# Performance work log

Hardware: AMD Instinct MI355X
Metric: run time of the kernel (lower is better)

Reference implementation:

```python
import jax, jax.numpy as jnp
import numpy as np

T = 5  # frames per clip, hardcoded in the module
H = 8  # heads


def _to_heads(z, b, n_, h, dh):
    # '(b t) n (h d) -> b h (n t) d' with t=T
    z = z.reshape(b, T, n_, h, dh)
    z = z.transpose(0, 3, 2, 1, 4)  # b h n t d
    return z.reshape(b, h, n_ * T, dh)


def _from_heads(z, b, n_, h, dh):
    # 'b h (n t) d -> (b t) n (h d)'
    z = z.reshape(b, h, n_, T, dh)
    z = z.transpose(0, 3, 2, 1, 4)  # b t n h d
    return z.reshape(b * T, n_, h * dh)


def setup_inputs() -> dict:
    key = jax.random.key(0)
    ks = jax.random.split(key, 6)
    bt, n, dim = 160, 257, 512
    inner = 512
    x = jax.random.normal(ks[0], (bt, n, dim), dtype=jnp.float32)
    mask = jax.random.uniform(ks[1], (bt, 16, 16), dtype=jnp.float32)
    Wv_qkv = jax.random.normal(ks[2], (dim, inner * 3), dtype=jnp.float32) * (dim ** -0.5)
    Wa_qkv = jax.random.normal(ks[3], (dim, inner * 3), dtype=jnp.float32) * (dim ** -0.5)
    Wo = jax.random.normal(ks[4], (inner, dim), dtype=jnp.float32) * (inner ** -0.5)
    bo = jnp.zeros((dim,), dtype=jnp.float32)
    return {"x": x, "mask": mask, "Wv_qkv": Wv_qkv, "Wa_qkv": Wa_qkv, "Wo": Wo, "bo": bo}


def reference(x, mask, Wv_qkv, Wa_qkv, Wo, bo):
    bt, n, dim = x.shape
    b = bt // T
    h = H
    inner = Wv_qkv.shape[1] // 3
    dh = inner // h
    scale = dh ** -0.5

    A = x[:, :1]   # (bt, 1, dim)
    V = x[:, 1:]   # (bt, n-1, dim)

    v_qkv = jnp.split(V @ Wv_qkv, 3, axis=-1)
    a_qkv = jnp.split(A @ Wa_qkv, 3, axis=-1)
    qv, kv, vv = (_to_heads(z, b, n - 1, h, dh) for z in v_qkv)  # (b,h,(n-1)*T,dh)
    qa, ka, va = (_to_heads(z, b, 1, h, dh) for z in a_qkv)       # (b,h,T,dh)

    # multiplicative query mask: (bt,16,16) -> (bt, n-1, 1) broadcast to dim -> heads layout
    m = jnp.broadcast_to(mask.reshape(bt, n - 1, 1), (bt, n - 1, h * dh))
    m = _to_heads(m, b, n - 1, h, dh)
    qv = qv * m

    # audio queries attend over visual keys/values
    av_dots = jnp.einsum('bhqd,bhkd->bhqk', qa, kv) * scale  # (b,h,T,(n-1)*T)
    av_out = jnp.einsum('bhqk,bhkd->bhqd', jax.nn.softmax(av_dots, axis=-1), vv)

    # visual queries attend over audio keys/values
    va_dots = jnp.einsum('bhqd,bhkd->bhqk', qv, ka) * scale  # (b,h,(n-1)*T,T)
    va_out = jnp.einsum('bhqk,bhkd->bhqd', jax.nn.softmax(va_dots, axis=-1), va)

    a_out = _from_heads(av_out, b, 1, h, dh)      # (bt, 1, inner)
    v_out = _from_heads(va_out, b, n - 1, h, dh)  # (bt, n-1, inner)
    out = jnp.concatenate((a_out, v_out), axis=1)  # (bt, n, inner)
    return out @ Wo + bo
```

## Files before the change

kernel.cpp:

```cpp
#include <hip/hip_runtime.h>
#include <hip/hip_bf16.h>

typedef unsigned short u16;
typedef __bf16 bf16x8 __attribute__((ext_vector_type(8)));
typedef u16 u16x8 __attribute__((ext_vector_type(8)));
typedef float f32x4 __attribute__((ext_vector_type(4)));

__device__ __forceinline__ float bf2f(u16 u) {
    return __uint_as_float(((unsigned)u) << 16);
}
__device__ __forceinline__ u16 f2bf(float f) {
    unsigned u = __float_as_uint(f);
    unsigned r = (u + 0x7fffu + ((u >> 16) & 1u)) >> 16;
    return (u16)r;
}

__device__ __forceinline__ void gl_lds16(const u16* g, u16* l) {
    __builtin_amdgcn_global_load_lds(
        (const __attribute__((address_space(1))) void*)g,
        (__attribute__((address_space(3))) void*)l, 16, 0, 0);
}

__global__ __launch_bounds__(256) void prep(const float* __restrict__ x,
                                            const float* __restrict__ Wv,
                                            const float* __restrict__ Wa,
                                            const float* __restrict__ Wo,
                                            u16* __restrict__ xb,
                                            u16* __restrict__ WvTv,
                                            u16* __restrict__ WaT,
                                            u16* __restrict__ WoT) {
    __shared__ float tile[64][65];
    int blk = blockIdx.x;
    if (blk < 10280) {
        int i = (blk * 256 + threadIdx.x) * 8;
        float4 a = *(const float4*)&x[i];
        float4 b = *(const float4*)&x[i + 4];
        u16x8 o;
        o[0] = f2bf(a.x); o[1] = f2bf(a.y); o[2] = f2bf(a.z); o[3] = f2bf(a.w);
        o[4] = f2bf(b.x); o[5] = f2bf(b.y); o[6] = f2bf(b.z); o[7] = f2bf(b.w);
        *(u16x8*)&xb[i] = o;
        return;
    }
    blk -= 10280;
    const float* W; u16* WT; int N, stride, coff;
    if (blk < 64)       { W = Wv; WT = WvTv; N = 512;  stride = 1536; coff = 1024; }
    else if (blk < 256) { W = Wa; WT = WaT;  N = 1536; stride = 1536; coff = 0; blk -= 64; }
    else                { W = Wo; WT = WoT;  N = 512;  stride = 512;  coff = 0; blk -= 256; }
    const int nt = N >> 6;
    const int k0 = (blk / nt) << 6;
    const int n0 = (blk % nt) << 6;
    for (int i = threadIdx.x; i < 4096; i += 256) {
        int r = i >> 6, c = i & 63;
        tile[r][c] = W[(size_t)(k0 + r) * stride + coff + n0 + c];
    }
    __syncthreads();
    for (int i = threadIdx.x; i < 4096; i += 256) {
        int r = i >> 6, c = i & 63;
        WT[(size_t)(n0 + r) * 512 + k0 + c] = f2bf(tile[c][r]);
    }
}

template <int MODE, int OUTF>
__global__ __launch_bounds__(256) void gemm_k(const u16* __restrict__ A,
                                              const u16* __restrict__ Bt,
                                              void* __restrict__ Cv,
                                              const float* __restrict__ bias,
                                              int M, int N, int K) {
    __shared__ u16 As[128][64];
    __shared__ u16 Bs[128][64];
    const int t = threadIdx.x;
    const int bn0 = blockIdx.x * 128;
    const int bm0 = blockIdx.y * 128;
    const int wave = t >> 6, lane = t & 63;
    const int wm = (wave >> 1) * 64, wn = (wave & 1) * 64;
    const int lr = lane & 15, lh = lane >> 4;
    const int srow = wave * 8 + (lane >> 3);
    const int scol = (lane & 7) * 8;

    f32x4 acc[4][4] = {};

    for (int kt = 0; kt < K; kt += 64) {
        __syncthreads();
#pragma unroll
        for (int i = 0; i < 4; i++) {
            int row = i * 32 + srow;
            int r = bm0 + row;
            long g;
            if (MODE == 0) g = (r < M) ? (long)r : 0l;
            else           g = (r < M) ? (long)r * 257 : 0l;
            gl_lds16(&A[g * K + kt + scol], &As[0][0] + i * 2048 + wave * 512);
            long nr = bn0 + row;
            gl_lds16(&Bt[nr * K + kt + scol], &Bs[0][0] + i * 2048 + wave * 512);
        }
        __syncthreads();
#pragma unroll
        for (int kk = 0; kk < 2; kk++) {
            bf16x8 af[4], bfr[4];
#pragma unroll
            for (int mi = 0; mi < 4; mi++)
                af[mi] = *(const bf16x8*)&As[wm + mi * 16 + lr][kk * 32 + lh * 8];
#pragma unroll
            for (int ni = 0; ni < 4; ni++)
                bfr[ni] = *(const bf16x8*)&Bs[wn + ni * 16 + lr][kk * 32 + lh * 8];
#pragma unroll
            for (int mi = 0; mi < 4; mi++)
#pragma unroll
                for (int ni = 0; ni < 4; ni++)
                    acc[mi][ni] = __builtin_amdgcn_mfma_f32_16x16x32_bf16(
                        af[mi], bfr[ni], acc[mi][ni], 0, 0, 0);
        }
    }

#pragma unroll
    for (int mi = 0; mi < 4; mi++)
#pragma unroll
        for (int ni = 0; ni < 4; ni++)
#pragma unroll
            for (int r2 = 0; r2 < 4; r2++) {
                int m = bm0 + wm + mi * 16 + lh * 4 + r2;
                if (m < M) {
                    int nc = bn0 + wn + ni * 16 + lr;
                    float v = acc[mi][ni][r2];
                    if (OUTF == 2)      ((float*)Cv)[(size_t)m * 257 * N + nc] = v + bias[nc];
                    else                ((u16*)Cv)[(size_t)m * N + nc] = f2bf(v);
                }
            }
}

__global__ __launch_bounds__(1024) void gemm_vs(const u16* __restrict__ A,
                                                const u16* __restrict__ WvTv,
                                                const u16* __restrict__ wcomb,
                                                u16* __restrict__ vv,
                                                float* __restrict__ pglob,
                                                float* __restrict__ vascore) {
    __shared__ u16 As[2][256][64];
    __shared__ u16 Bs[2][256][64];
    const int t = threadIdx.x;
    const int nwg = gridDim.x;
    const int orig = blockIdx.x;
    const int qc = nwg >> 3;
    const int xcd = orig & 7, slot = orig >> 3;
    const int wgid = xcd * qc + slot;
    const int my = wgid / 3, sec = wgid % 3;
    const int bm0 = my * 256;
    const int bt = my, b = bt / 5, t5 = bt - b * 5;
    const int bn0 = (sec < 2) ? sec * 256 : 0;
    const u16* Bt = (sec < 2) ? WvTv : (wcomb + (size_t)b * 256 * 512);
    const int wave = t >> 6, lane = t & 63;
    const int wm = (wave >> 2) * 64, wn = (wave & 3) * 64;
    const int lr = lane & 15, lh = lane >> 4;
    const int xr = (lr & 7) << 3;
    const bool active = (sec < 2) || (wn < 128);
    u16* AsF = &As[0][0][0];
    u16* BsF = &Bs[0][0][0];

    const int gsa = ((lane & 7) ^ (lane >> 3)) * 8;
    auto stage = [&](int buf, int kt_) {
        const int kc = kt_ * 64;
#pragma unroll
        for (int j = 0; j < 2; j++) {
            int c0 = j * 1024 + wave * 64;
            int row = (c0 + lane) >> 3;
            int r = bm0 + row;
            long ga = (long)(r >> 8) * 257 + (r & 255) + 1;
            gl_lds16(&A[ga * 512 + kc + gsa], AsF + buf * 16384 + c0 * 8);
            gl_lds16(&Bt[(long)(bn0 + row) * 512 + kc + gsa], BsF + buf * 16384 + c0 * 8);
        }
    };

    f32x4 acc[4][4] = {};

    stage(0, 0);
    __builtin_amdgcn_sched_barrier(0);
    stage(1, 1);
    __builtin_amdgcn_sched_barrier(0);
    asm volatile("s_waitcnt vmcnt(0)" ::: "memory");
    __builtin_amdgcn_s_barrier();
    __builtin_amdgcn_sched_barrier(0);

    int cur = 0;
    for (int kt = 0; kt < 8; kt++) {
        if (active) {
            __builtin_amdgcn_s_setprio(1);
#pragma unroll
            for (int kk = 0; kk < 2; kk++) {
                bf16x8 af[4], bfr[4];
#pragma unroll
                for (int mi = 0; mi < 4; mi++)
                    af[mi] = *(const bf16x8*)&As[cur][wm + mi * 16 + lr][(kk * 32 + lh * 8) ^ xr];
#pragma unroll
                for (int ni = 0; ni < 4; ni++)
                    bfr[ni] = *(const bf16x8*)&Bs[cur][wn + ni * 16 + lr][(kk * 32 + lh * 8) ^ xr];
#pragma unroll
                for (int mi = 0; mi < 4; mi++)
#pragma unroll
                    for (int ni = 0; ni < 4; ni++)
                        acc[mi][ni] = __builtin_amdgcn_mfma_f32_16x16x32_bf16(
                            af[mi], bfr[ni], acc[mi][ni], 0, 0, 0);
            }
            __builtin_amdgcn_s_setprio(0);
        }
        if (kt == 7) break;
        __builtin_amdgcn_sched_barrier(0);
        __builtin_amdgcn_s_barrier();
        __builtin_amdgcn_sched_barrier(0);
        if (kt + 2 < 8) {
            stage(cur, kt + 2);
            __builtin_amdgcn_sched_barrier(0);
            asm volatile("s_waitcnt vmcnt(4)" ::: "memory");
        } else {
            asm volatile("s_waitcnt vmcnt(0)" ::: "memory");
        }
        __builtin_amdgcn_sched_barrier(0);
        __builtin_amdgcn_s_barrier();
        __builtin_amdgcn_sched_barrier(0);
        cur ^= 1;
    }

    if (sec < 2) {
#pragma unroll
        for (int mi = 0; mi < 4; mi++)
#pragma unroll
            for (int ni = 0; ni < 4; ni++)
#pragma unroll
                for (int r2 = 0; r2 < 4; r2++) {
                    int m = bm0 + wm + mi * 16 + lh * 4 + r2;
                    int nc = bn0 + wn + ni * 16 + lr;
                    vv[(size_t)m * 512 + nc] = f2bf(acc[mi][ni][r2]);
                }
    } else {
#pragma unroll
        for (int ni = 0; ni < 4; ni++) {
            const int c = wn + ni * 16 + lr;
            if (c < 40) {
                const int h = c / 5, q = c - h * 5;
                float* prow = &pglob[((size_t)(b * 8 + h) * 5 + q) * 1280];
#pragma unroll
                for (int mi = 0; mi < 4; mi++)
#pragma unroll
                    for (int r2 = 0; r2 < 4; r2++) {
                        int m = bm0 + wm + mi * 16 + lh * 4 + r2;
                        int j = m & 255;
                        prow[j * 5 + t5] = acc[mi][ni][r2];
                    }
            } else if (c < 80) {
#pragma unroll
                for (int mi = 0; mi < 4; mi++)
#pragma unroll
                    for (int r2 = 0; r2 < 4; r2++) {
                        int m = bm0 + wm + mi * 16 + lh * 4 + r2;
                        vascore[(size_t)m * 40 + (c - 40)] = acc[mi][ni][r2];
                    }
            }
        }
    }
}

__global__ __launch_bounds__(512) void wbuild_all(const float* __restrict__ Wv,
                                                  const float* __restrict__ Wo,
                                                  const u16* __restrict__ aqkv,
                                                  u16* __restrict__ wcomb,
                                                  u16* __restrict__ vob) {
    const int blk = blockIdx.x;
    const int t = threadIdx.x;
    if (blk < 128) {
        __shared__ float avec[20][64];
        const int kind = blk & 1, h = (blk >> 1) & 7, vc = blk >> 4;
        const int v0 = vc * 20;
        const int aoff = (kind == 0) ? 0 : 512;
        for (int i = t; i < 1280; i += 512) {
            int vi = i >> 6, d = i & 63;
            int v = v0 + vi, b = v / 5, q = v - b * 5;
            avec[vi][d] = bf2f(aqkv[(size_t)(b * 5 + q) * 1536 + aoff + h * 64 + d]);
        }
        const int k = t;
        const int colbase = (kind == 0) ? (512 + h * 64) : (h * 64);
        float wr[64];
#pragma unroll
        for (int d = 0; d < 64; d += 4) {
            float4 w4 = *(const float4*)&Wv[(size_t)k * 1536 + colbase + d];
            wr[d] = w4.x; wr[d + 1] = w4.y; wr[d + 2] = w4.z; wr[d + 3] = w4.w;
        }
        __syncthreads();
        for (int vi = 0; vi < 20; vi++) {
            float acc = 0.f;
#pragma unroll
            for (int d = 0; d < 64; d++) acc += wr[d] * avec[vi][d];
            int v = v0 + vi, b = v / 5, q = v - b * 5;
            int c = kind * 40 + h * 5 + q;
            wcomb[((size_t)b * 256 + c) * 512 + k] = f2bf(acc);
        }
        return;
    }
    if (blk < 160) {
        const int b = blk - 128;
        const size_t base = (size_t)b * 256 * 512 + 80 * 512;
        u16x8 z = {};
        for (int i = t * 8; i < 24576; i += 4096)
            *(u16x8*)&wcomb[base + i] = z;
        return;
    }
    {
        __shared__ float vaL[5][64];
        const int bh = blk - 160;
        const int b = bh >> 3, h = bh & 7;
        for (int i = t; i < 320; i += 512) {
            int q = i >> 6, d = i & 63;
            vaL[q][d] = bf2f(aqkv[(size_t)(b * 5 + q) * 1536 + 1024 + h * 64 + d]);
        }
        __syncthreads();
        const int c = t;
        float a0 = 0, a1 = 0, a2 = 0, a3 = 0, a4 = 0;
#pragma unroll 8
        for (int d = 0; d < 64; d++) {
            float w = Wo[(size_t)(h * 64 + d) * 512 + c];
            a0 += w * vaL[0][d];
            a1 += w * vaL[1][d];
            a2 += w * vaL[2][d];
            a3 += w * vaL[3][d];
            a4 += w * vaL[4][d];
        }
        const size_t base = ((size_t)b * 512 + c) * 64;
        vob[base + h * 5]     = f2bf(a0);
        vob[base + h * 5 + 1] = f2bf(a1);
        vob[base + h * 5 + 2] = f2bf(a2);
        vob[base + h * 5 + 3] = f2bf(a3);
        vob[base + h * 5 + 4] = f2bf(a4);
        if (h == 0) {
#pragma unroll
            for (int i = 40; i < 64; i++) vob[base + i] = 0;
        }
    }
}

__global__ __launch_bounds__(256) void vaout(const float* __restrict__ vascore,
                                             const float* __restrict__ mask,
                                             const u16* __restrict__ vob,
                                             const float* __restrict__ bo,
                                             float* __restrict__ out) {
    __shared__ u16 As[128][64];
    __shared__ u16 Bs[128][64];
    const int blk = blockIdx.x;
    const int nh = blk & 3, mh = (blk >> 2) & 1, bt = blk >> 3;
    const int b = bt / 5;
    const int t = threadIdx.x;
    if (t < 128) {
        const int rr = mh * 128 + t;
        const size_t m = (size_t)bt * 256 + rr;
        const float mval = mask[m] * 0.125f;
        const float* sp = &vascore[m * 40];
        u16 prow[64];
#pragma unroll
        for (int h = 0; h < 8; h++) {
            float r0 = sp[h * 5] * mval, r1 = sp[h * 5 + 1] * mval, r2 = sp[h * 5 + 2] * mval;
            float r3 = sp[h * 5 + 3] * mval, r4 = sp[h * 5 + 4] * mval;
            float mx = fmaxf(fmaxf(fmaxf(r0, r1), fmaxf(r2, r3)), r4);
            float e0 = __expf(r0 - mx), e1 = __expf(r1 - mx), e2 = __expf(r2 - mx);
            float e3 = __expf(r3 - mx), e4 = __expf(r4 - mx);
            float inv = 1.f / (e0 + e1 + e2 + e3 + e4);
            prow[h * 5]     = f2bf(e0 * inv);
            prow[h * 5 + 1] = f2bf(e1 * inv);
            prow[h * 5 + 2] = f2bf(e2 * inv);
            prow[h * 5 + 3] = f2bf(e3 * inv);
            prow[h * 5 + 4] = f2bf(e4 * inv);
        }
#pragma unroll
        for (int i = 40; i < 64; i++) prow[i] = 0;
#pragma unroll
        for (int s = 0; s < 8; s++)
            *(u16x8*)&As[t][s * 8] = *(u16x8*)&prow[s * 8];
    }
    for (int i = t; i < 1024; i += 256) {
        int r = i >> 3, seg = i & 7;
        *(u16x8*)&Bs[r][seg * 8] =
            *(const u16x8*)&vob[((size_t)b * 512 + nh * 128 + r) * 64 + seg * 8];
    }
    __syncthreads();

    const int wave = t >> 6, lane = t & 63;
    const int wm = (wave >> 1) * 64, wn = (wave & 1) * 64;
    const int lr = lane & 15, lh = lane >> 4;
    f32x4 acc[4][4] = {};
#pragma unroll
    for (int kk = 0; kk < 2; kk++) {
        bf16x8 af[4], bfr[4];
#pragma unroll
        for (int mi = 0; mi < 4; mi++)
            af[mi] = *(const bf16x8*)&As[wm + mi * 16 + lr][kk * 32 + lh * 8];
#pragma unroll
        for (int ni = 0; ni < 4; ni++)
            bfr[ni] = *(const bf16x8*)&Bs[wn + ni * 16 + lr][kk * 32 + lh * 8];
#pragma unroll
        for (int mi = 0; mi < 4; mi++)
#pragma unroll
            for (int ni = 0; ni < 4; ni++)
                acc[mi][ni] = __builtin_amdgcn_mfma_f32_16x16x32_bf16(
                    af[mi], bfr[ni], acc[mi][ni], 0, 0, 0);
    }

    const size_t obase = ((size_t)bt * 257 + 1 + mh * 128) * 512 + nh * 128;
#pragma unroll
    for (int mi = 0; mi < 4; mi++)
#pragma unroll
        for (int ni = 0; ni < 4; ni++)
#pragma unroll
            for (int r2 = 0; r2 < 4; r2++) {
                int row = wm + mi * 16 + lh * 4 + r2;
                int col = wn + ni * 16 + lr;
                out[obase + (size_t)row * 512 + col] = acc[mi][ni][r2] + bo[nh * 128 + col];
            }
}

__global__ __launch_bounds__(1024) void av_finish(const u16* __restrict__ vv,
                                                  const float* __restrict__ pglob,
                                                  u16* __restrict__ catA) {
    __shared__ float pl[5][1280];
    __shared__ float pbuf[16][5][64];
    const int bh = blockIdx.x;
    const int bi = bh >> 3, hd = bh & 7;
    const int t = threadIdx.x;
    for (int i = t; i < 6400; i += 1024) {
        pl[0][i] = pglob[(size_t)bh * 6400 + i] * 0.125f;
    }
    __syncthreads();
    const int wave = t >> 6, lane = t & 63;
    if (wave < 5) {
        float v[20];
        float mx = -3.4e38f;
#pragma unroll
        for (int i = 0; i < 20; i++) {
            v[i] = pl[wave][lane + i * 64];
            mx = fmaxf(mx, v[i]);
        }
#pragma unroll
        for (int off = 32; off > 0; off >>= 1) mx = fmaxf(mx, __shfl_xor(mx, off));
        float sum = 0.f;
#pragma unroll
        for (int i = 0; i < 20; i++) {
            v[i] = __expf(v[i] - mx);
            sum += v[i];
        }
#pragma unroll
        for (int off = 32; off > 0; off >>= 1) sum += __shfl_xor(sum, off);
        const float inv = 1.f / sum;
#pragma unroll
        for (int i = 0; i < 20; i++) pl[wave][lane + i * 64] = v[i] * inv;
    }
    __syncthreads();
    {
        float a0 = 0, a1 = 0, a2 = 0, a3 = 0, a4 = 0;
        const int j0 = wave * 16;
        for (int jj = 0; jj < 16; jj++) {
            const int j = j0 + jj;
#pragma unroll
            for (int t5 = 0; t5 < 5; t5++) {
                float v = bf2f(vv[(size_t)((bi * 5 + t5) * 256 + j) * 512 + hd * 64 + lane]);
                const int s = j * 5 + t5;
                a0 += pl[0][s] * v;
                a1 += pl[1][s] * v;
                a2 += pl[2][s] * v;
                a3 += pl[3][s] * v;
                a4 += pl[4][s] * v;
            }
        }
        pbuf[wave][0][lane] = a0;
        pbuf[wave][1][lane] = a1;
        pbuf[wave][2][lane] = a2;
        pbuf[wave][3][lane] = a3;
        pbuf[wave][4][lane] = a4;
    }
    __syncthreads();
    if (t < 320) {
        const int q = t >> 6, d = t & 63;
        float s = 0.f;
#pragma unroll
        for (int w = 0; w < 16; w++) s += pbuf[w][q][d];
        catA[(size_t)(bi * 5 + q) * 512 + hd * 64 + d] = f2bf(s);
    }
}

extern "C" void kernel_launch(void* const* d_in, const int* in_sizes, int n_in,
                              void* d_out, int out_size, void* d_ws, size_t ws_size,
                              hipStream_t stream) {
    const float* x    = (const float*)d_in[0];
    const float* mask = (const float*)d_in[1];
    const float* Wv   = (const float*)d_in[2];
    const float* Wa   = (const float*)d_in[3];
    const float* Wo   = (const float*)d_in[4];
    const float* bo   = (const float*)d_in[5];
    float* out = (float*)d_out;

    char* ws = (char*)d_ws;
    u16*   xb      = (u16*)(ws);
    u16*   WvTv    = (u16*)(ws + 42106880);
    u16*   WaT     = (u16*)(ws + 42631168);
    u16*   WoT     = (u16*)(ws + 44204032);
    u16*   aqkv    = (u16*)(ws + 44728320);
    u16*   wcomb   = (u16*)(ws + 45219840);
    u16*   vv      = (u16*)(ws + 53608448);
    float* vascore = (float*)(ws + 95551488);
    float* pglob   = (float*)(ws + 102105088);
    u16*   catA    = (u16*)(ws + 108658688);
    u16*   vob     = (u16*)(ws + 109969408);

    prep<<<dim3(10600), 256, 0, stream>>>(x, Wv, Wa, Wo, xb, WvTv, WaT, WoT);

    gemm_k<2, 0><<<dim3(12, 2), 256, 0, stream>>>(xb, WaT, aqkv, nullptr, 160, 1536, 512);

    wbuild_all<<<dim3(416), 512, 0, stream>>>(Wv, Wo, aqkv, wcomb, vob);

    gemm_vs<<<dim3(480), 1024, 0, stream>>>(xb, WvTv, wcomb, vv, pglob, vascore);

    vaout<<<dim3(1280), 256, 0, stream>>>(vascore, mask, vob, bo, out);

    av_finish<<<dim3(256), 1024, 0, stream>>>(vv, pglob, catA);

    gemm_k<0, 2><<<dim3(4, 2), 256, 0, stream>>>(catA, WoT, out, bo, 160, 512, 512);
}
```

Measured before the change: 158.4 us.

## Compute audio QKV projection inside prep and drop separate GEMM and zero-fill

The audio-token QKV projection is now computed directly in the prep kernel with per-thread fp32 dot products over the Wa columns. This removes the Wa transpose, the separate gemm_k launch and the aqkv round trip from a dedicated kernel. The wcomb zero-fill blocks are removed from wbuild_all, and the per-wave 'active' guard in gemm_vs is dropped, so idle waves now issue MFMAs on unzeroed wcomb rows whose results are presumably discarded. The trade-off is fewer launches and less setup work in exchange for extra MFMA work in gemm_vs and cache-heavy scalar loads of Wa in prep.

```diff
diff --git a/kernel.cpp b/kernel.cpp
--- a/kernel.cpp
+++ b/kernel.cpp
@@ -27,12 +27,12 @@
                                             const float* __restrict__ Wo,
                                             u16* __restrict__ xb,
                                             u16* __restrict__ WvTv,
-                                            u16* __restrict__ WaT,
-                                            u16* __restrict__ WoT) {
-    __shared__ float tile[64][65];
+                                            u16* __restrict__ WoT,
+                                            u16* __restrict__ aqkv) {
     int blk = blockIdx.x;
+    const int t = threadIdx.x;
     if (blk < 10280) {
-        int i = (blk * 256 + threadIdx.x) * 8;
+        int i = (blk * 256 + t) * 8;
         float4 a = *(const float4*)&x[i];
         float4 b = *(const float4*)&x[i + 4];
         u16x8 o;
@@ -42,21 +42,42 @@
         return;
     }
     blk -= 10280;
-    const float* W; u16* WT; int N, stride, coff;
-    if (blk < 64)       { W = Wv; WT = WvTv; N = 512;  stride = 1536; coff = 1024; }
-    else if (blk < 256) { W = Wa; WT = WaT;  N = 1536; stride = 1536; coff = 0; blk -= 64; }
-    else                { W = Wo; WT = WoT;  N = 512;  stride = 512;  coff = 0; blk -= 256; }
-    const int nt = N >> 6;
-    const int k0 = (blk / nt) << 6;
-    const int n0 = (blk % nt) << 6;
-    for (int i = threadIdx.x; i < 4096; i += 256) {
-        int r = i >> 6, c = i & 63;
-        tile[r][c] = W[(size_t)(k0 + r) * stride + coff + n0 + c];
-    }
-    __syncthreads();
-    for (int i = threadIdx.x; i < 4096; i += 256) {
-        int r = i >> 6, c = i & 63;
-        WT[(size_t)(n0 + r) * 512 + k0 + c] = f2bf(tile[c][r]);
+    if (blk < 128) {
+        __shared__ float tile[64][65];
+        const float* W; u16* WT; int N, stride, coff;
+        if (blk < 64) { W = Wv; WT = WvTv; N = 512; stride = 1536; coff = 1024; }
+        else          { W = Wo; WT = WoT;  N = 512; stride = 512;  coff = 0; blk -= 64; }
+        const int nt = N >> 6;
+        const int k0 = (blk / nt) << 6;
+        const int n0 = (blk % nt) << 6;
+        for (int i = t; i < 4096; i += 256) {
+            int r = i >> 6, c = i & 63;
+            tile[r][c] = W[(size_t)(k0 + r) * stride + coff + n0 + c];
+        }
+        __syncthreads();
+        for (int i = t; i < 4096; i += 256) {
+            int r = i >> 6, c = i & 63;
+            WT[(size_t)(n0 + r) * 512 + k0 + c] = f2bf(tile[c][r]);
+        }
+        return;
+    }
+    {
+        __shared__ float xrow[512];
+        const int a = blk - 128;
+        const int tok = a / 3, s = a - tok * 3;
+        const int colbase = s * 512;
+        const float* xr = x + (size_t)tok * 257 * 512;
+        for (int i = t; i < 512; i += 256) xrow[i] = xr[i];
+        __syncthreads();
+#pragma unroll
+        for (int cc = 0; cc < 2; cc++) {
+            const int c = colbase + cc * 256 + t;
+            float acc = 0.f;
+#pragma unroll 8
+            for (int k = 0; k < 512; k++)
+                acc += Wa[(size_t)k * 1536 + c] * xrow[k];
+            aqkv[(size_t)tok * 1536 + c] = f2bf(acc);
+        }
     }
 }
 
@@ -121,8 +142,8 @@
                 if (m < M) {
                     int nc = bn0 + wn + ni * 16 + lr;
                     float v = acc[mi][ni][r2];
-                    if (OUTF == 2)      ((float*)Cv)[(size_t)m * 257 * N + nc] = v + bias[nc];
-                    else                ((u16*)Cv)[(size_t)m * N + nc] = f2bf(v);
+                    if (OUTF == 2) ((float*)Cv)[(size_t)m * 257 * N + nc] = v + bias[nc];
+                    else           ((u16*)Cv)[(size_t)m * N + nc] = f2bf(v);
                 }
             }
 }
@@ -150,7 +171,6 @@
     const int wm = (wave >> 2) * 64, wn = (wave & 3) * 64;
     const int lr = lane & 15, lh = lane >> 4;
     const int xr = (lr & 7) << 3;
-    const bool active = (sec < 2) || (wn < 128);
     u16* AsF = &As[0][0][0];
     u16* BsF = &Bs[0][0][0];
 
@@ -180,26 +200,24 @@
 
     int cur = 0;
     for (int kt = 0; kt < 8; kt++) {
-        if (active) {
-            __builtin_amdgcn_s_setprio(1);
-#pragma unroll
-            for (int kk = 0; kk < 2; kk++) {
-                bf16x8 af[4], bfr[4];
-#pragma unroll
-                for (int mi = 0; mi < 4; mi++)
-                    af[mi] = *(const bf16x8*)&As[cur][wm + mi * 16 + lr][(kk * 32 + lh * 8) ^ xr];
+        __builtin_amdgcn_s_setprio(1);
+#pragma unroll
+        for (int kk = 0; kk < 2; kk++) {
+            bf16x8 af[4], bfr[4];
+#pragma unroll
+            for (int mi = 0; mi < 4; mi++)
+                af[mi] = *(const bf16x8*)&As[cur][wm + mi * 16 + lr][(kk * 32 + lh * 8) ^ xr];
+#pragma unroll
+            for (int ni = 0; ni < 4; ni++)
+                bfr[ni] = *(const bf16x8*)&Bs[cur][wn + ni * 16 + lr][(kk * 32 + lh * 8) ^ xr];
+#pragma unroll
+            for (int mi = 0; mi < 4; mi++)
 #pragma unroll
                 for (int ni = 0; ni < 4; ni++)
-                    bfr[ni] = *(const bf16x8*)&Bs[cur][wn + ni * 16 + lr][(kk * 32 + lh * 8) ^ xr];
-#pragma unroll
-                for (int mi = 0; mi < 4; mi++)
-#pragma unroll
-                    for (int ni = 0; ni < 4; ni++)
-                        acc[mi][ni] = __builtin_amdgcn_mfma_f32_16x16x32_bf16(
-                            af[mi], bfr[ni], acc[mi][ni], 0, 0, 0);
-            }
-            __builtin_amdgcn_s_setprio(0);
-        }
+                    acc[mi][ni] = __builtin_amdgcn_mfma_f32_16x16x32_bf16(
+                        af[mi], bfr[ni], acc[mi][ni], 0, 0, 0);
+        }
+        __builtin_amdgcn_s_setprio(0);
         if (kt == 7) break;
         __builtin_amdgcn_sched_barrier(0);
         __builtin_amdgcn_s_barrier();
@@ -292,17 +310,9 @@
         }
         return;
     }
-    if (blk < 160) {
-        const int b = blk - 128;
-        const size_t base = (size_t)b * 256 * 512 + 80 * 512;
-        u16x8 z = {};
-        for (int i = t * 8; i < 24576; i += 4096)
-            *(u16x8*)&wcomb[base + i] = z;
-        return;
-    }
     {
         __shared__ float vaL[5][64];
-        const int bh = blk - 160;
+        const int bh = blk - 128;
         const int b = bh >> 3, h = bh & 7;
         for (int i = t; i < 320; i += 512) {
             int q = i >> 6, d = i & 63;
@@ -493,21 +503,18 @@
     char* ws = (char*)d_ws;
     u16*   xb      = (u16*)(ws);
     u16*   WvTv    = (u16*)(ws + 42106880);
-    u16*   WaT     = (u16*)(ws + 42631168);
-    u16*   WoT     = (u16*)(ws + 44204032);
-    u16*   aqkv    = (u16*)(ws + 44728320);
-    u16*   wcomb   = (u16*)(ws + 45219840);
-    u16*   vv      = (u16*)(ws + 53608448);
-    float* vascore = (float*)(ws + 95551488);
-    float* pglob   = (float*)(ws + 102105088);
-    u16*   catA    = (u16*)(ws + 108658688);
-    u16*   vob     = (u16*)(ws + 109969408);
-
-    prep<<<dim3(10600), 256, 0, stream>>>(x, Wv, Wa, Wo, xb, WvTv, WaT, WoT);
-
-    gemm_k<2, 0><<<dim3(12, 2), 256, 0, stream>>>(xb, WaT, aqkv, nullptr, 160, 1536, 512);
-
-    wbuild_all<<<dim3(416), 512, 0, stream>>>(Wv, Wo, aqkv, wcomb, vob);
+    u16*   WoT     = (u16*)(ws + 42631168);
+    u16*   aqkv    = (u16*)(ws + 43155456);
+    u16*   wcomb   = (u16*)(ws + 43646976);
+    u16*   vv      = (u16*)(ws + 52035584);
+    float* vascore = (float*)(ws + 93978624);
+    float* pglob   = (float*)(ws + 100532224);
+    u16*   catA    = (u16*)(ws + 107085824);
+    u16*   vob     = (u16*)(ws + 108396544);
+
+    prep<<<dim3(10888), 256, 0, stream>>>(x, Wv, Wa, Wo, xb, WvTv, WoT, aqkv);
+
+    wbuild_all<<<dim3(384), 512, 0, stream>>>(Wv, Wo, aqkv, wcomb, vob);
 
     gemm_vs<<<dim3(480), 1024, 0, stream>>>(xb, WvTv, wcomb, vv, pglob, vascore);
 
```

Result: slower. 191.3 us (+20.7%).
